# Kernel optimization log

Measured on AMD Instinct MI355X. Metric: run time of the kernel, lower is better.

The kernel has to match this reference:

```python
import jax, jax.numpy as jnp
import numpy as np

B, S, H, E, K = 4, 4096, 2048, 64, 8
SEQ_ALPHA = 0.01


def setup_inputs() -> dict:
    key = jax.random.key(0)
    k1, k2 = jax.random.split(key)
    x = jax.random.normal(k1, (B, S, H), dtype=jnp.float32)
    # kaiming_uniform_(a=sqrt(5)) on [E, H] -> bound = 1/sqrt(H)
    bound = 1.0 / np.sqrt(H)
    weight = jax.random.uniform(k2, (E, H), dtype=jnp.float32, minval=-bound, maxval=bound)
    expert_bias = jnp.zeros((E,), dtype=jnp.float32)
    return {"x": x, "weight": weight, "expert_bias": expert_bias}


def reference(x, weight, expert_bias):
    bsz, seq_len, _ = x.shape
    x_flat = x.reshape(-1, x.shape[-1])                      # [T, H], T = B*S
    logits = x_flat @ weight.T                               # [T, E]
    scores = jax.nn.sigmoid(logits)
    biased_logits = logits + expert_bias[None, :]
    _, topk_idx = jax.lax.top_k(biased_logits, K)            # [T, K] int32
    topk_w = jnp.take_along_axis(scores, topk_idx, axis=-1)  # [T, K]
    topk_w = topk_w / (topk_w.sum(axis=-1, keepdims=True) + 1e-10)  # K > 1
    # load stats (training-mode bincount)
    expert_load = jnp.bincount(topk_idx.reshape(-1), length=E).astype(jnp.int64)
    # sequence-wise balance loss (DeepSeek-V3)
    scores_r = scores.reshape(bsz, seq_len, E)
    expert_mask = jax.nn.one_hot(topk_idx.reshape(bsz, -1), E, dtype=scores.dtype)  # [B, S*K, E]
    f_i = expert_mask.sum(axis=1) / (K * seq_len)            # [B, E]
    normalized = scores_r / (scores_r.sum(axis=2, keepdims=True) + 1e-10)
    P_i = normalized.mean(axis=1)                            # [B, E]
    aux_seq_loss = SEQ_ALPHA * (f_i * P_i).sum(axis=1).mean()
    return (topk_idx, topk_w, aux_seq_loss, expert_load)
```

## Files before the change

### kernel.cpp

```cpp
#include <hip/hip_runtime.h>
#include <math.h>

#define HDIM 2048
#define TTOK 16384
#define NEXP 64
#define TOPK 8
#define SLEN 4096
#define NBATCH 4
#define PARTSZ (NEXP * TTOK)

#define OFF_W    131072
#define OFF_LOSS 262144
#define OFF_LOAD 262145

#define WS_PACC 0
#define WS_CACC 256
#define WS_CNT  512
#define WS_WT   1024
#define WS_PART (1024 + HDIM * NEXP)

__global__ __launch_bounds__(256) void transpose_w(const float* __restrict__ W,
                                                   float* __restrict__ Wt) {
  __shared__ float tile[64][65];
  const int tid = threadIdx.x;
  const int k0 = blockIdx.x * 64;
  {
    const int kc = (tid & 15) << 2;
    const int er = tid >> 4;
#pragma unroll
    for (int i = 0; i < 4; ++i) {
      int e = er + i * 16;
      float4 v = *(const float4*)(W + (size_t)e * HDIM + k0 + kc);
      tile[e][kc + 0] = v.x; tile[e][kc + 1] = v.y;
      tile[e][kc + 2] = v.z; tile[e][kc + 3] = v.w;
    }
  }
  __syncthreads();
  {
    const int e4 = (tid & 15) << 2;
    const int kr = tid >> 4;
#pragma unroll
    for (int i = 0; i < 4; ++i) {
      int k = kr + i * 16;
      float4 v;
      v.x = tile[e4 + 0][k]; v.y = tile[e4 + 1][k];
      v.z = tile[e4 + 2][k]; v.w = tile[e4 + 3][k];
      *(float4*)(Wt + (size_t)(k0 + k) * NEXP + e4) = v;
    }
  }
}

template <int KS>
__global__ __launch_bounds__(512, 8) void gate_gemm(
    const float* __restrict__ x,
    const float* __restrict__ Wt,
    float* __restrict__ part) {
  constexpr int KR = HDIM / KS;
  constexpr int NT = KR / 32;
  __shared__ float xs[2][128 * 32];

  const int tid = threadIdx.x;
  const int lane = tid & 63;
  const int wv = __builtin_amdgcn_readfirstlane(tid >> 6);
  const int eg = wv & 3;
  const int th = wv >> 2;
  const int bid = blockIdx.x;
  const int kh = bid & (KS - 1);
  const int tg = bid >> (KS == 8 ? 3 : 2);
  const int tok0 = tg << 7;
  const int kb = kh * KR;

  float acc[16];
#pragma unroll
  for (int j = 0; j < 16; ++j) acc[j] = 0.f;

  const int r0 = tid >> 3;
  const int sg = tid & 7;
  const int sslot = (sg ^ (r0 & 7)) << 2;
  const float* xp0 = x + (size_t)(tok0 + r0) * HDIM + kb + (sg << 2);
  const float* xp1 = xp0 + (size_t)64 * HDIM;
  float4 a0 = *(const float4*)xp0;
  float4 a1 = *(const float4*)xp1;

  const int myrow = (th << 6) + lane;
  const int rbase = myrow << 5;
  const int rs = lane & 7;

  for (int kt = 0; kt < NT; ++kt) {
    float* xb = &xs[kt & 1][0];
    *(float4*)&xb[(r0 << 5) + sslot] = a0;
    *(float4*)&xb[((r0 + 64) << 5) + sslot] = a1;
    __syncthreads();
    if (kt + 1 < NT) {
      a0 = *(const float4*)(xp0 + ((kt + 1) << 5));
      a1 = *(const float4*)(xp1 + ((kt + 1) << 5));
    }
    const float* wkb = Wt + ((size_t)(kb + (kt << 5)) << 6) + (eg << 4);
#pragma unroll
    for (int c = 0; c < 8; ++c) {
      float4 xv = *(const float4*)&xb[rbase + ((c ^ rs) << 2)];
      const float xf[4] = {xv.x, xv.y, xv.z, xv.w};
#pragma unroll
      for (int q = 0; q < 4; ++q) {
        const float* wr = wkb + (((c << 2) + q) << 6);
#pragma unroll
        for (int j = 0; j < 16; ++j) acc[j] = fmaf(xf[q], wr[j], acc[j]);
      }
    }
  }

  float* dst = part + (size_t)kh * PARTSZ + ((size_t)(eg << 4)) * TTOK + tok0 +
               (th << 6) + lane;
#pragma unroll
  for (int j = 0; j < 16; ++j) dst[(size_t)j * TTOK] = acc[j];
}

template <int KS>
__global__ __launch_bounds__(128) void gate_epilogue(
    const float* __restrict__ part, const float* __restrict__ bias,
    float* __restrict__ out, float* __restrict__ Pacc,
    float* __restrict__ Cacc, int* __restrict__ counter) {
  __shared__ float le[64][65];
  __shared__ float rinv_sh[64];
  __shared__ unsigned csum[64];
  __shared__ int lastf;

  const int tid = threadIdx.x;
  const int t0 = blockIdx.x << 6;

  if (tid < 64) csum[tid] = 0u;

#pragma unroll
  for (int w = 0; w < 8; ++w) {
    const int f = (w << 7) + tid;
    const int e = f >> 4;
    const int q = f & 15;
    const float* p = part + (size_t)e * TTOK + t0 + (q << 2);
    float4 v[KS];
#pragma unroll
    for (int s = 0; s < KS; ++s) v[s] = *(const float4*)(p + (size_t)s * PARTSZ);
    float4 r;
    if (KS == 8) {
      r.x = ((v[0].x + v[1].x) + (v[2].x + v[3].x)) + ((v[4].x + v[5].x) + (v[6].x + v[7].x));
      r.y = ((v[0].y + v[1].y) + (v[2].y + v[3].y)) + ((v[4].y + v[5].y) + (v[6].y + v[7].y));
      r.z = ((v[0].z + v[1].z) + (v[2].z + v[3].z)) + ((v[4].z + v[5].z) + (v[6].z + v[7].z));
      r.w = ((v[0].w + v[1].w) + (v[2].w + v[3].w)) + ((v[4].w + v[5].w) + (v[6].w + v[7].w));
    } else {
      r.x = (v[0].x + v[1].x) + (v[2].x + v[3].x);
      r.y = (v[0].y + v[1].y) + (v[2].y + v[3].y);
      r.z = (v[0].z + v[1].z) + (v[2].z + v[3].z);
      r.w = (v[0].w + v[1].w) + (v[2].w + v[3].w);
    }
    le[e][(q << 2) + 0] = r.x; le[e][(q << 2) + 1] = r.y;
    le[e][(q << 2) + 2] = r.z; le[e][(q << 2) + 3] = r.w;
  }
  __syncthreads();

  if (tid < 64) {
    float bl[64];
    float ssum = 0.f;
#pragma unroll
    for (int e = 0; e < NEXP; ++e) {
      float l = le[e][tid];
      ssum += 1.f / (1.f + expf(-l));
      bl[e] = l + bias[e];
    }
    rinv_sh[tid] = 1.f / (ssum + 1e-10f);

    unsigned long long chosen = 0ull;
    int i8[TOPK];
    float w8[TOPK];
    float wsum = 0.f;
#pragma unroll
    for (int j = 0; j < TOPK; ++j) {
      float best = -1e30f;
      int bi = 0;
      float braw = 0.f;
#pragma unroll
      for (int e = 0; e < NEXP; ++e) {
        bool ok = (((chosen >> e) & 1ull) == 0ull) && (bl[e] > best);
        if (ok) { best = bl[e]; bi = e; braw = bl[e] - bias[e]; }
      }
      chosen |= (1ull << bi);
      float sc = 1.f / (1.f + expf(-braw));
      i8[j] = bi;
      w8[j] = sc;
      wsum += sc;
    }
    const float inv = 1.f / (wsum + 1e-10f);
    const int t = t0 + tid;
    float4 o;
    o.x = (float)i8[0]; o.y = (float)i8[1]; o.z = (float)i8[2]; o.w = (float)i8[3];
    *(float4*)(out + (size_t)t * TOPK) = o;
    o.x = (float)i8[4]; o.y = (float)i8[5]; o.z = (float)i8[6]; o.w = (float)i8[7];
    *(float4*)(out + (size_t)t * TOPK + 4) = o;
    o.x = w8[0] * inv; o.y = w8[1] * inv; o.z = w8[2] * inv; o.w = w8[3] * inv;
    *(float4*)(out + OFF_W + (size_t)t * TOPK) = o;
    o.x = w8[4] * inv; o.y = w8[5] * inv; o.z = w8[6] * inv; o.w = w8[7] * inv;
    *(float4*)(out + OFF_W + (size_t)t * TOPK + 4) = o;
#pragma unroll
    for (int j = 0; j < TOPK; ++j) atomicAdd(&csum[i8[j]], 1u);
  }
  __syncthreads();

  const int b = blockIdx.x >> 6;
  if (tid < 64) {
    float p = 0.f;
    for (int tt = 0; tt < 64; ++tt) {
      float sc = 1.f / (1.f + expf(-le[tid][tt]));
      p += sc * rinv_sh[tt];
    }
    atomicAdd(&Pacc[(b << 6) + tid], p);
    atomicAdd(&Cacc[(b << 6) + tid], (float)csum[tid]);
  }
  __syncthreads();
  __threadfence();
  if (tid == 0) {
    int old = __hip_atomic_fetch_add(counter, 1, __ATOMIC_ACQ_REL,
                                     __HIP_MEMORY_SCOPE_AGENT);
    lastf = (old == 255) ? 1 : 0;
  }
  __syncthreads();

  if (lastf && tid < 64) {
    const int e = tid;
    float load = 0.f, partl = 0.f;
#pragma unroll
    for (int bb = 0; bb < NBATCH; ++bb) {
      float c = __hip_atomic_load(&Cacc[(bb << 6) + e], __ATOMIC_RELAXED,
                                  __HIP_MEMORY_SCOPE_AGENT);
      float p = __hip_atomic_load(&Pacc[(bb << 6) + e], __ATOMIC_RELAXED,
                                  __HIP_MEMORY_SCOPE_AGENT);
      load += c;
      partl += (c * (1.f / (TOPK * (float)SLEN))) * (p * (1.f / (float)SLEN));
    }
    out[OFF_LOAD + e] = load;
#pragma unroll
    for (int off = 32; off; off >>= 1) partl += __shfl_down(partl, off);
    if (e == 0) out[OFF_LOSS] = 0.01f * partl * (1.f / (float)NBATCH);
  }
}

extern "C" void kernel_launch(void* const* d_in, const int* in_sizes, int n_in,
                              void* d_out, int out_size, void* d_ws, size_t ws_size,
                              hipStream_t stream) {
  const float* x = (const float*)d_in[0];
  const float* W = (const float*)d_in[1];
  const float* bias = (const float*)d_in[2];
  float* out = (float*)d_out;

  float* ws = (float*)d_ws;
  float* Pacc = ws + WS_PACC;
  float* Cacc = ws + WS_CACC;
  int* counter = (int*)(ws + WS_CNT);
  float* Wt = ws + WS_WT;
  float* part = ws + WS_PART;

  hipMemsetAsync(ws, 0, WS_WT * sizeof(float), stream);
  transpose_w<<<32, 256, 0, stream>>>(W, Wt);

  const size_t need8 = ((size_t)WS_PART + 8 * (size_t)PARTSZ) * sizeof(float);
  if (ws_size >= need8) {
    gate_gemm<8><<<1024, 512, 0, stream>>>(x, Wt, part);
    gate_epilogue<8><<<256, 128, 0, stream>>>(part, bias, out, Pacc, Cacc, counter);
  } else {
    gate_gemm<4><<<512, 512, 0, stream>>>(x, Wt, part);
    gate_epilogue<4><<<256, 128, 0, stream>>>(part, bias, out, Pacc, Cacc, counter);
  }
}
```

Before: 268.0 us.

## Fuse gate GEMM and routing epilogue into one kernel without split-K

Replaces the split-K gate GEMM and its separate reduction/epilogue kernel with a single kernel. Each block computes full-K logits for 64 tokens, with each wave owning 8 experts. Logits and sigmoids go into shared memory, and top-k, the normalised weights, load counts and sequence-loss partials are computed in the same block. This removes the partial-sum workspace traffic and one launch. In exchange the grid drops to 256 blocks with 8 accumulators per lane, so parallelism and per-thread arithmetic intensity are lower.

```diff
diff --git a/kernel.cpp b/kernel.cpp
--- a/kernel.cpp
+++ b/kernel.cpp
@@ -7,7 +7,6 @@
 #define TOPK 8
 #define SLEN 4096
 #define NBATCH 4
-#define PARTSZ (NEXP * TTOK)
 
 #define OFF_W    131072
 #define OFF_LOSS 262144
@@ -17,7 +16,6 @@
 #define WS_CACC 256
 #define WS_CNT  512
 #define WS_WT   1024
-#define WS_PART (1024 + HDIM * NEXP)
 
 __global__ __launch_bounds__(256) void transpose_w(const float* __restrict__ W,
                                                    float* __restrict__ Wt) {
@@ -50,52 +48,50 @@
   }
 }
 
-template <int KS>
-__global__ __launch_bounds__(512, 8) void gate_gemm(
+__global__ __launch_bounds__(512) void gate_fused(
     const float* __restrict__ x,
     const float* __restrict__ Wt,
-    float* __restrict__ part) {
-  constexpr int KR = HDIM / KS;
-  constexpr int NT = KR / 32;
-  __shared__ float xs[2][128 * 32];
+    const float* __restrict__ bias,
+    float* __restrict__ out, float* __restrict__ Pacc,
+    float* __restrict__ Cacc, int* __restrict__ counter) {
+  __shared__ float xs[2][64 * 32];
+  __shared__ float le[64 * 65];
+  __shared__ float sgm[64 * 65];
+  __shared__ float rsum[8 * 64];
+  __shared__ float rinvs[64];
+  __shared__ float biasl[64];
+  __shared__ unsigned csum[64];
+  __shared__ int lastf;
 
   const int tid = threadIdx.x;
   const int lane = tid & 63;
   const int wv = __builtin_amdgcn_readfirstlane(tid >> 6);
-  const int eg = wv & 3;
-  const int th = wv >> 2;
-  const int bid = blockIdx.x;
-  const int kh = bid & (KS - 1);
-  const int tg = bid >> (KS == 8 ? 3 : 2);
-  const int tok0 = tg << 7;
-  const int kb = kh * KR;
-
-  float acc[16];
-#pragma unroll
-  for (int j = 0; j < 16; ++j) acc[j] = 0.f;
+  const int tok0 = blockIdx.x << 6;
+
+  if (tid < 64) { csum[tid] = 0u; biasl[tid] = bias[tid]; }
 
   const int r0 = tid >> 3;
-  const int sg = tid & 7;
-  const int sslot = (sg ^ (r0 & 7)) << 2;
-  const float* xp0 = x + (size_t)(tok0 + r0) * HDIM + kb + (sg << 2);
-  const float* xp1 = xp0 + (size_t)64 * HDIM;
-  float4 a0 = *(const float4*)xp0;
-  float4 a1 = *(const float4*)xp1;
-
-  const int myrow = (th << 6) + lane;
-  const int rbase = myrow << 5;
+  const int sgr = tid & 7;
+  const int sslot = (sgr ^ (r0 & 7)) << 2;
+  const float* xp = x + (size_t)(tok0 + r0) * HDIM + (sgr << 2);
+  float4 aA = *(const float4*)xp;
+  float4 aB = *(const float4*)(xp + 32);
+
+  const int rbase = lane << 5;
   const int rs = lane & 7;
-
+  float acc[8];
+#pragma unroll
+  for (int j = 0; j < 8; ++j) acc[j] = 0.f;
+  const float* wb = Wt + (wv << 3);
+
+  constexpr int NT = HDIM / 32;
   for (int kt = 0; kt < NT; ++kt) {
     float* xb = &xs[kt & 1][0];
-    *(float4*)&xb[(r0 << 5) + sslot] = a0;
-    *(float4*)&xb[((r0 + 64) << 5) + sslot] = a1;
+    *(float4*)&xb[(r0 << 5) + sslot] = aA;
     __syncthreads();
-    if (kt + 1 < NT) {
-      a0 = *(const float4*)(xp0 + ((kt + 1) << 5));
-      a1 = *(const float4*)(xp1 + ((kt + 1) << 5));
-    }
-    const float* wkb = Wt + ((size_t)(kb + (kt << 5)) << 6) + (eg << 4);
+    aA = aB;
+    if (kt + 2 < NT) aB = *(const float4*)(xp + ((kt + 2) << 5));
+    const float* wkb = wb + ((size_t)(kt << 5) << 6);
 #pragma unroll
     for (int c = 0; c < 8; ++c) {
       float4 xv = *(const float4*)&xb[rbase + ((c ^ rs) << 2)];
@@ -104,68 +100,32 @@
       for (int q = 0; q < 4; ++q) {
         const float* wr = wkb + (((c << 2) + q) << 6);
 #pragma unroll
-        for (int j = 0; j < 16; ++j) acc[j] = fmaf(xf[q], wr[j], acc[j]);
+        for (int j = 0; j < 8; ++j) acc[j] = fmaf(xf[q], wr[j], acc[j]);
       }
     }
   }
 
-  float* dst = part + (size_t)kh * PARTSZ + ((size_t)(eg << 4)) * TTOK + tok0 +
-               (th << 6) + lane;
-#pragma unroll
-  for (int j = 0; j < 16; ++j) dst[(size_t)j * TTOK] = acc[j];
-}
-
-template <int KS>
-__global__ __launch_bounds__(128) void gate_epilogue(
-    const float* __restrict__ part, const float* __restrict__ bias,
-    float* __restrict__ out, float* __restrict__ Pacc,
-    float* __restrict__ Cacc, int* __restrict__ counter) {
-  __shared__ float le[64][65];
-  __shared__ float rinv_sh[64];
-  __shared__ unsigned csum[64];
-  __shared__ int lastf;
-
-  const int tid = threadIdx.x;
-  const int t0 = blockIdx.x << 6;
-
-  if (tid < 64) csum[tid] = 0u;
-
-#pragma unroll
-  for (int w = 0; w < 8; ++w) {
-    const int f = (w << 7) + tid;
-    const int e = f >> 4;
-    const int q = f & 15;
-    const float* p = part + (size_t)e * TTOK + t0 + (q << 2);
-    float4 v[KS];
-#pragma unroll
-    for (int s = 0; s < KS; ++s) v[s] = *(const float4*)(p + (size_t)s * PARTSZ);
-    float4 r;
-    if (KS == 8) {
-      r.x = ((v[0].x + v[1].x) + (v[2].x + v[3].x)) + ((v[4].x + v[5].x) + (v[6].x + v[7].x));
-      r.y = ((v[0].y + v[1].y) + (v[2].y + v[3].y)) + ((v[4].y + v[5].y) + (v[6].y + v[7].y));
-      r.z = ((v[0].z + v[1].z) + (v[2].z + v[3].z)) + ((v[4].z + v[5].z) + (v[6].z + v[7].z));
-      r.w = ((v[0].w + v[1].w) + (v[2].w + v[3].w)) + ((v[4].w + v[5].w) + (v[6].w + v[7].w));
-    } else {
-      r.x = (v[0].x + v[1].x) + (v[2].x + v[3].x);
-      r.y = (v[0].y + v[1].y) + (v[2].y + v[3].y);
-      r.z = (v[0].z + v[1].z) + (v[2].z + v[3].z);
-      r.w = (v[0].w + v[1].w) + (v[2].w + v[3].w);
-    }
-    le[e][(q << 2) + 0] = r.x; le[e][(q << 2) + 1] = r.y;
-    le[e][(q << 2) + 2] = r.z; le[e][(q << 2) + 3] = r.w;
-  }
-  __syncthreads();
-
-  if (tid < 64) {
+  {
+    float rs8 = 0.f;
+    const int lrow = lane * 65 + (wv << 3);
+#pragma unroll
+    for (int j = 0; j < 8; ++j) {
+      float s = 1.f / (1.f + expf(-acc[j]));
+      le[lrow + j] = acc[j];
+      sgm[lrow + j] = s;
+      rs8 += s;
+    }
+    rsum[(wv << 6) + lane] = rs8;
+  }
+  __syncthreads();
+
+  const int b = (int)(blockIdx.x >> 6);
+
+  if (wv == 0) {
+    const int t = lane;
     float bl[64];
-    float ssum = 0.f;
-#pragma unroll
-    for (int e = 0; e < NEXP; ++e) {
-      float l = le[e][tid];
-      ssum += 1.f / (1.f + expf(-l));
-      bl[e] = l + bias[e];
-    }
-    rinv_sh[tid] = 1.f / (ssum + 1e-10f);
+#pragma unroll
+    for (int e = 0; e < NEXP; ++e) bl[e] = le[t * 65 + e] + biasl[e];
 
     unsigned long long chosen = 0ull;
     int i8[TOPK];
@@ -175,44 +135,42 @@
     for (int j = 0; j < TOPK; ++j) {
       float best = -1e30f;
       int bi = 0;
-      float braw = 0.f;
 #pragma unroll
       for (int e = 0; e < NEXP; ++e) {
         bool ok = (((chosen >> e) & 1ull) == 0ull) && (bl[e] > best);
-        if (ok) { best = bl[e]; bi = e; braw = bl[e] - bias[e]; }
+        if (ok) { best = bl[e]; bi = e; }
       }
       chosen |= (1ull << bi);
-      float sc = 1.f / (1.f + expf(-braw));
+      float sc = sgm[t * 65 + bi];
       i8[j] = bi;
       w8[j] = sc;
       wsum += sc;
     }
     const float inv = 1.f / (wsum + 1e-10f);
-    const int t = t0 + tid;
+    const int tt = tok0 + t;
     float4 o;
     o.x = (float)i8[0]; o.y = (float)i8[1]; o.z = (float)i8[2]; o.w = (float)i8[3];
-    *(float4*)(out + (size_t)t * TOPK) = o;
+    *(float4*)(out + (size_t)tt * TOPK) = o;
     o.x = (float)i8[4]; o.y = (float)i8[5]; o.z = (float)i8[6]; o.w = (float)i8[7];
-    *(float4*)(out + (size_t)t * TOPK + 4) = o;
+    *(float4*)(out + (size_t)tt * TOPK + 4) = o;
     o.x = w8[0] * inv; o.y = w8[1] * inv; o.z = w8[2] * inv; o.w = w8[3] * inv;
-    *(float4*)(out + OFF_W + (size_t)t * TOPK) = o;
+    *(float4*)(out + OFF_W + (size_t)tt * TOPK) = o;
     o.x = w8[4] * inv; o.y = w8[5] * inv; o.z = w8[6] * inv; o.w = w8[7] * inv;
-    *(float4*)(out + OFF_W + (size_t)t * TOPK + 4) = o;
+    *(float4*)(out + OFF_W + (size_t)tt * TOPK + 4) = o;
 #pragma unroll
     for (int j = 0; j < TOPK; ++j) atomicAdd(&csum[i8[j]], 1u);
-  }
-  __syncthreads();
-
-  const int b = blockIdx.x >> 6;
-  if (tid < 64) {
+    atomicAdd(&Cacc[(b << 6) + lane], (float)csum[lane]);
+  } else if (wv == 1) {
+    const int t = lane;
+    float ss = 0.f;
+#pragma unroll
+    for (int w = 0; w < 8; ++w) ss += rsum[(w << 6) + t];
+    rinvs[t] = 1.f / (ss + 1e-10f);
     float p = 0.f;
-    for (int tt = 0; tt < 64; ++tt) {
-      float sc = 1.f / (1.f + expf(-le[tid][tt]));
-      p += sc * rinv_sh[tt];
-    }
-    atomicAdd(&Pacc[(b << 6) + tid], p);
-    atomicAdd(&Cacc[(b << 6) + tid], (float)csum[tid]);
-  }
+    for (int t2 = 0; t2 < 64; ++t2) p += sgm[t2 * 65 + lane] * rinvs[t2];
+    atomicAdd(&Pacc[(b << 6) + lane], p);
+  }
+
   __syncthreads();
   __threadfence();
   if (tid == 0) {
@@ -254,17 +212,8 @@
   float* Cacc = ws + WS_CACC;
   int* counter = (int*)(ws + WS_CNT);
   float* Wt = ws + WS_WT;
-  float* part = ws + WS_PART;
 
   hipMemsetAsync(ws, 0, WS_WT * sizeof(float), stream);
   transpose_w<<<32, 256, 0, stream>>>(W, Wt);
-
-  const size_t need8 = ((size_t)WS_PART + 8 * (size_t)PARTSZ) * sizeof(float);
-  if (ws_size >= need8) {
-    gate_gemm<8><<<1024, 512, 0, stream>>>(x, Wt, part);
-    gate_epilogue<8><<<256, 128, 0, stream>>>(part, bias, out, Pacc, Cacc, counter);
-  } else {
-    gate_gemm<4><<<512, 512, 0, stream>>>(x, Wt, part);
-    gate_epilogue<4><<<256, 128, 0, stream>>>(part, bias, out, Pacc, Cacc, counter);
-  }
+  gate_fused<<<256, 512, 0, stream>>>(x, Wt, bias, out, Pacc, Cacc, counter);
 }
```

Measured after the change: 350.4 us. 30.8% more time.
